# Kernel optimization log

Measured on AMD Instinct MI355X. Metric: run time of the kernel, lower is better.

The kernel has to match this reference:

```python
import jax, jax.numpy as jnp
import numpy as np

NUM_HEADS = 16
TOP_K = 64


def setup_inputs() -> dict:
    key = jax.random.key(0)
    ks = jax.random.split(key, 9)
    B, S, E = 2, 1024, 1024
    x = jax.random.normal(ks[0], (B, S, E), jnp.float32)
    init = lambda k: jax.random.normal(k, (E, E), jnp.float32) * 0.02
    return {
        "x": x,
        "Wq": init(ks[1]), "bq": jnp.zeros((E,), jnp.float32),
        "Wk": init(ks[2]), "bk": jnp.zeros((E,), jnp.float32),
        "Wv": init(ks[3]), "bv": jnp.zeros((E,), jnp.float32),
        "Wo": init(ks[4]), "bo": jnp.zeros((E,), jnp.float32),
    }


def reference(x, Wq, bq, Wk, bk, Wv, bv, Wo, bo):
    B, S, E = x.shape
    H = NUM_HEADS
    hd = E // H
    scale = jnp.sqrt(jnp.float32(hd))

    def proj(W, b):  # torch nn.Linear: y = x @ W^T + b -> [B,H,S,hd]
        return (x @ W.T + b).reshape(B, S, H, hd).transpose(0, 2, 1, 3)

    q = proj(Wq, bq)
    k = proj(Wk, bk)
    v = proj(Wv, bv)

    # full scores, then per-query top-k selection (same math as the torch per-i loop)
    scores = jnp.einsum('bhqd,bhkd->bhqk', q, k) / scale          # [B,H,S,S]
    top_scores, top_idx = jax.lax.top_k(scores, TOP_K)            # [B,H,S,K]

    # gather top-k values: vg[b,h,q,j,:] = v[b,h, top_idx[b,h,q,j], :]
    vg = jnp.take_along_axis(v[:, :, None, :, :], top_idx[..., None], axis=3)  # [B,H,S,K,hd]

    # torch recomputes q . gathered_k / scale, which equals top_scores exactly
    w = jax.nn.softmax(top_scores, axis=-1)                       # [B,H,S,K]
    out = jnp.einsum('bhqk,bhqkd->bhqd', w, vg)                   # [B,H,S,hd]

    out = out.transpose(0, 2, 1, 3).reshape(B, S, E)
    return out @ Wo.T + bo
```

## Files before the change

kernel.cpp:

```cpp
#include <hip/hip_runtime.h>
#include <hip/hip_bf16.h>
#include <stdint.h>


typedef __bf16 bf16_t;
typedef bf16_t bf16x8 __attribute__((ext_vector_type(8)));
typedef bf16_t bf16x4 __attribute__((ext_vector_type(4)));
typedef float  f32x4  __attribute__((ext_vector_type(4)));

#define NB 2
#define SS 1024
#define EE 1024
#define NH 16
#define HD 64
#define NBH (NB*NH)
#define NX_ ((size_t)NB*SS*EE)
#define NW_ ((size_t)EE*EE)

__device__ __forceinline__ f32x4 mfma16(bf16x8 a, bf16x8 b, f32x4 c) {
  return __builtin_amdgcn_mfma_f32_16x16x32_bf16(a, b, c, 0, 0, 0);
}

__device__ __forceinline__ void split3(float x, bf16_t& h, bf16_t& m, bf16_t& l) {
  h = (bf16_t)x;
  float r = x - (float)h;
  m = (bf16_t)r;
  float r2 = r - (float)m;
  l = (bf16_t)r2;
}

__device__ __forceinline__ void wave_fence() {
  __builtin_amdgcn_wave_barrier();
  __builtin_amdgcn_s_waitcnt(0);
  __builtin_amdgcn_wave_barrier();
}

__device__ __forceinline__ void gld16(const bf16_t* g, bf16_t* l) {
  __builtin_amdgcn_global_load_lds(
      (const __attribute__((address_space(1))) void*)g,
      (__attribute__((address_space(3))) void*)l, 16, 0, 0);
}

__global__ __launch_bounds__(256) void presplit_all(
    const float* __restrict__ x,  const float* __restrict__ wq,
    const float* __restrict__ wk, const float* __restrict__ wv,
    const float* __restrict__ wo, bf16_t* __restrict__ base)
{
  const int blk = blockIdx.x;
  const float* src; bf16_t* h; size_t n; int i;
  if (blk < 2048)      { src = x;  h = base;                   n = NX_; i = blk;        }
  else if (blk < 3072) { src = wq; h = base + 3*NX_;           n = NW_; i = blk - 2048; }
  else if (blk < 4096) { src = wk; h = base + 3*NX_ + 3*NW_;   n = NW_; i = blk - 3072; }
  else if (blk < 5120) { src = wv; h = base + 3*NX_ + 6*NW_;   n = NW_; i = blk - 4096; }
  else                 { src = wo; h = base + 3*NX_ + 9*NW_;   n = NW_; i = blk - 5120; }
  bf16_t* m = h + n;
  bf16_t* l = m + n;
  int idx = i * 256 + threadIdx.x;
  float4 v = ((const float4*)src)[idx];
  float t[4] = { v.x, v.y, v.z, v.w };
  bf16x4 hv, mv, lv;
#pragma unroll
  for (int j = 0; j < 4; j++) {
    bf16_t a, b, c;
    split3(t[j], a, b, c);
    hv[j] = a; mv[j] = b; lv[j] = c;
  }
  ((bf16x4*)h)[idx] = hv;
  ((bf16x4*)m)[idx] = mv;
  ((bf16x4*)l)[idx] = lv;
}

__global__ __launch_bounds__(256, 2) void gemm_qk(
    const bf16_t* __restrict__ Ah, const bf16_t* __restrict__ Am,
    const bf16_t* __restrict__ Al,
    const bf16_t* __restrict__ Bqh, const bf16_t* __restrict__ Bqm,
    const bf16_t* __restrict__ Bql,
    const bf16_t* __restrict__ Bkh, const bf16_t* __restrict__ Bkm,
    const bf16_t* __restrict__ Bkl,
    const float* __restrict__ biasq, const float* __restrict__ biask,
    bf16_t* __restrict__ qH, bf16_t* __restrict__ qM, bf16_t* __restrict__ qL,
    bf16_t* __restrict__ kH, bf16_t* __restrict__ kM, bf16_t* __restrict__ kL)
{
  __shared__ bf16_t As[3][128 * 32];
  __shared__ bf16_t Bs[3][64 * 32];

  const int z = blockIdx.z;
  const bf16_t* AP[3] = { Ah, Am, Al };
  const bf16_t* BP[3] = { z ? Bkh : Bqh, z ? Bkm : Bqm, z ? Bkl : Bql };
  const float* bias = z ? biask : biasq;
  bf16_t* dH = z ? kH : qH;
  bf16_t* dM = z ? kM : qM;
  bf16_t* dL = z ? kL : qL;

  const int tid  = threadIdx.x;
  const int wv   = tid >> 6, lane = tid & 63;
  const int quad = lane >> 4, l16 = lane & 15;
  const int m0 = blockIdx.y * 128, n0 = blockIdx.x * 64;
  const int wm = (wv & 1) * 64, wn = (wv >> 1) * 32;

  const int arow = wv * 32 + (lane >> 2);
  const int brow = wv * 16 + (lane >> 2);
  const int q8   = (lane & 3) * 8;
  const size_t aoff0 = (size_t)(m0 + arow) * 1024 + q8;
  const size_t boff  = (size_t)(n0 + brow) * 1024 + q8;

  f32x4 accH0[4][2] = {};
  f32x4 accH1[4][2] = {};
  f32x4 accC [4][2] = {};

  for (int k0 = 0; k0 < 1024; k0 += 32) {
    __syncthreads();
#pragma unroll
    for (int L = 0; L < 3; L++) {
      gld16(AP[L] + aoff0 + k0,              &As[L][(wv * 32) * 32]);
      gld16(AP[L] + aoff0 + 16 * 1024 + k0,  &As[L][(wv * 32 + 16) * 32]);
      gld16(BP[L] + boff + k0,               &Bs[L][(wv * 16) * 32]);
    }
    __syncthreads();

    bf16x8 bfr[2][3];
#pragma unroll
    for (int nt = 0; nt < 2; nt++)
#pragma unroll
      for (int L = 0; L < 3; L++)
        bfr[nt][L] = *(const bf16x8*)&Bs[L][(wn + nt * 16 + l16) * 32 + quad * 8];

    const bool hi = (k0 >= 512);
#pragma unroll
    for (int mt = 0; mt < 4; mt++) {
      bf16x8 af[3];
#pragma unroll
      for (int L = 0; L < 3; L++)
        af[L] = *(const bf16x8*)&As[L][(wm + mt * 16 + l16) * 32 + quad * 8];
#pragma unroll
      for (int nt = 0; nt < 2; nt++) {
        f32x4& H = hi ? accH1[mt][nt] : accH0[mt][nt];
        H = mfma16(af[0], bfr[nt][0], H);
        f32x4 c = accC[mt][nt];
        c = mfma16(af[0], bfr[nt][1], c);
        c = mfma16(af[1], bfr[nt][0], c);
        c = mfma16(af[0], bfr[nt][2], c);
        c = mfma16(af[2], bfr[nt][0], c);
        c = mfma16(af[1], bfr[nt][1], c);
        accC[mt][nt] = c;
      }
    }
  }

#pragma unroll
  for (int mt = 0; mt < 4; mt++)
#pragma unroll
  for (int nt = 0; nt < 2; nt++)
#pragma unroll
  for (int r  = 0; r  < 4;  r++) {
    int gm = m0 + wm + mt * 16 + quad * 4 + r;
    int gn = n0 + wn + nt * 16 + l16;
    float v = (accH0[mt][nt][r] + accH1[mt][nt][r]) + accC[mt][nt][r] + bias[gn];
    int b_ = gm >> 10, s_ = gm & 1023, h_ = gn >> 6, d_ = gn & 63;
    size_t di = (((size_t)b_ * NH + h_) * SS + s_) * HD + d_;
    bf16_t hh, mm, ll;
    split3(v, hh, mm, ll);
    dH[di] = hh; dM[di] = mm; dL[di] = ll;
  }
}

template<int MODE>
__global__ __launch_bounds__(256, 4) void gemm_nl2(
    const bf16_t* __restrict__ Ah, const bf16_t* __restrict__ Am,
    const bf16_t* __restrict__ Bh, const bf16_t* __restrict__ Bm,
    const float* __restrict__ bias, float* __restrict__ dF)
{
  __shared__ bf16_t As[2][64 * 32];
  __shared__ bf16_t Bs[2][64 * 32];

  const bf16_t* AP[2] = { Ah, Am };
  const bf16_t* BP[2] = { Bh, Bm };

  const int tid  = threadIdx.x;
  const int wv   = tid >> 6, lane = tid & 63;
  const int quad = lane >> 4, l16 = lane & 15;
  const int m0 = blockIdx.y * 64, n0 = blockIdx.x * 64;
  const int wm = (wv & 1) * 32, wn = (wv >> 1) * 32;

  const int srow = wv * 16 + (lane >> 2);
  const int q8   = (lane & 3) * 8;
  const size_t aoff = (size_t)(m0 + srow) * 1024 + q8;
  const size_t boff = (size_t)(n0 + srow) * 1024 + q8;

  f32x4 accH0[2][2] = {};
  f32x4 accH1[2][2] = {};
  f32x4 accC [2][2] = {};

  for (int k0 = 0; k0 < 1024; k0 += 32) {
    __syncthreads();
#pragma unroll
    for (int L = 0; L < 2; L++) {
      gld16(AP[L] + aoff + k0, &As[L][(wv * 16) * 32]);
      gld16(BP[L] + boff + k0, &Bs[L][(wv * 16) * 32]);
    }
    __syncthreads();

    bf16x8 bfr[2][2];
#pragma unroll
    for (int nt = 0; nt < 2; nt++)
#pragma unroll
      for (int L = 0; L < 2; L++)
        bfr[nt][L] = *(const bf16x8*)&Bs[L][(wn + nt * 16 + l16) * 32 + quad * 8];

    const bool hi = (k0 >= 512);
#pragma unroll
    for (int mt = 0; mt < 2; mt++) {
      bf16x8 af[2];
#pragma unroll
      for (int L = 0; L < 2; L++)
        af[L] = *(const bf16x8*)&As[L][(wm + mt * 16 + l16) * 32 + quad * 8];
#pragma unroll
      for (int nt = 0; nt < 2; nt++) {
        f32x4& H = hi ? accH1[mt][nt] : accH0[mt][nt];
        H = mfma16(af[0], bfr[nt][0], H);
        f32x4 c = accC[mt][nt];
        c = mfma16(af[0], bfr[nt][1], c);
        c = mfma16(af[1], bfr[nt][0], c);
        accC[mt][nt] = c;
      }
    }
  }

#pragma unroll
  for (int mt = 0; mt < 2; mt++)
#pragma unroll
  for (int nt = 0; nt < 2; nt++)
#pragma unroll
  for (int r  = 0; r  < 4;  r++) {
    int gm = m0 + wm + mt * 16 + quad * 4 + r;
    int gn = n0 + wn + nt * 16 + l16;
    float v = (accH0[mt][nt][r] + accH1[mt][nt][r]) + accC[mt][nt][r] + bias[gn];
    if (MODE == 2) {
      dF[(size_t)gm * 1024 + gn] = v;
    } else {
      int b_ = gm >> 10, s_ = gm & 1023, h_ = gn >> 6, d_ = gn & 63;
      dF[(((size_t)b_ * NH + h_) * SS + s_) * HD + d_] = v;
    }
  }
}

__global__ __launch_bounds__(1024, 4) void attn_topk(
    const bf16_t* __restrict__ qhg, const bf16_t* __restrict__ qmg,
    const bf16_t* __restrict__ qlg,
    const bf16_t* __restrict__ khg, const bf16_t* __restrict__ kmg,
    const bf16_t* __restrict__ klg,
    const float*  __restrict__ vg,
    bf16_t* __restrict__ attnH, bf16_t* __restrict__ attnM)
{
  __shared__ float  sc[16 * 516];
  __shared__ float  selW[16 * 64];
  __shared__ ushort selI[16 * 64];

  const int tid  = threadIdx.x;
  const int wv   = tid >> 6, lane = tid & 63;
  const int quad = lane >> 4, l16 = lane & 15;
  const int xcd = blockIdx.x & 7;
  const int g   = blockIdx.x >> 3;
  const int bh  = xcd + 8 * (g >> 6);
  const int qt  = g & 63;
  const int b_ = bh >> 4, h_ = bh & 15;
  const int q0 = qt * 16;

  const uint32_t qbase = ((uint32_t)bh * SS + q0 + l16) * HD + quad * 8;
  bf16x8 aH[2], aM[2], aL[2];
#pragma unroll
  for (int ks = 0; ks < 2; ks++) {
    aH[ks] = *(const bf16x8*)(qhg + qbase + ks * 32);
    aM[ks] = *(const bf16x8*)(qmg + qbase + ks * 32);
    aL[ks] = *(const bf16x8*)(qlg + qbase + ks * 32);
  }

  float fv[16];
#pragma unroll
  for (int c = 0; c < 2; c++) {
    const uint32_t kwb = ((uint32_t)bh * SS + c * 512 + wv * 32 + l16) * HD + quad * 8;
#pragma unroll
    for (int t2 = 0; t2 < 2; t2++) {
      const uint32_t kb = kwb + (uint32_t)t2 * 16 * HD;
      f32x4 accH = {}, accC = {};
      {
        bf16x8 bH = *(const bf16x8*)(khg + kb);
        bf16x8 bM = *(const bf16x8*)(kmg + kb);
        bf16x8 bL = *(const bf16x8*)(klg + kb);
        accH = mfma16(aH[0], bH, accH);
        accC = mfma16(aH[0], bM, accC);
        accC = mfma16(aM[0], bH, accC);
        accC = mfma16(aH[0], bL, accC);
        accC = mfma16(aL[0], bH, accC);
        accC = mfma16(aM[0], bM, accC);
      }
      {
        bf16x8 bH = *(const bf16x8*)(khg + kb + 32);
        bf16x8 bM = *(const bf16x8*)(kmg + kb + 32);
        bf16x8 bL = *(const bf16x8*)(klg + kb + 32);
        accH = mfma16(aH[1], bH, accH);
        accC = mfma16(aH[1], bM, accC);
        accC = mfma16(aM[1], bH, accC);
        accC = mfma16(aH[1], bL, accC);
        accC = mfma16(aL[1], bH, accC);
        accC = mfma16(aM[1], bM, accC);
      }
      int key = wv * 32 + t2 * 16 + l16;
#pragma unroll
      for (int r = 0; r < 4; r++)
        sc[(quad * 4 + r) * 516 + key] = (accH[r] + accC[r]) * 0.125f;
    }
    __syncthreads();
#pragma unroll
    for (int i = 0; i < 8; i++)
      fv[c * 8 + i] = sc[wv * 516 + i * 64 + lane];
    __syncthreads();
  }

  uint32_t* bins  = (uint32_t*)sc + wv * 516;
  float*    candV = (float*)bins;
  ushort*   candI = (ushort*)(bins + 64);

  const uint64_t lt = (1ull << lane) - 1ull;
  const int q = wv;
  {
    *(uint4*)(bins + lane * 8)     = uint4{0, 0, 0, 0};
    *(uint4*)(bins + lane * 8 + 4) = uint4{0, 0, 0, 0};
    wave_fence();
#pragma unroll
    for (int i = 0; i < 16; i++) {
      int b = (int)fmaxf(0.f, fminf(511.f, fmaf(fv[i], 32.f, 256.f)));
      atomicAdd(bins + b, 1u);
    }
    wave_fence();
    int base = 504 - 8 * lane;
    uint4 h0 = *(const uint4*)(bins + base);
    uint4 h1 = *(const uint4*)(bins + base + 4);
    uint32_t s_l = h0.x + h0.y + h0.z + h0.w + h1.x + h1.y + h1.z + h1.w;
    uint32_t x = s_l;
#pragma unroll
    for (int off = 1; off < 64; off <<= 1) {
      uint32_t y = __shfl_up(x, off);
      if (lane >= off) x += y;
    }
    uint32_t P = x - s_l;
    uint32_t harr[8] = { h1.w, h1.z, h1.y, h1.x, h0.w, h0.z, h0.y, h0.x };
    uint32_t cb = P, G = 0;
    int foundc = -1;
#pragma unroll
    for (int c = 0; c < 8; c++) {
      uint32_t hc = harr[c];
      if (foundc < 0 && (int)cb < 64 && (int)(cb + hc) >= 64) { foundc = c; G = cb; }
      cb += hc;
    }
    uint64_t fm = __ballot(foundc >= 0);
    int src   = __ffsll((unsigned long long)fm) - 1;
    int Bstar = __shfl((foundc >= 0) ? (511 - 8 * lane - foundc) : 0, src);
    int Gs    = __shfl((int)G, src);
    int needed = 64 - Gs;
    wave_fence();

    int pos = 0, cT = 0;
#pragma unroll
    for (int i = 0; i < 16; i++) {
      int b = (int)fmaxf(0.f, fminf(511.f, fmaf(fv[i], 32.f, 256.f)));
      bool hi = b > Bstar;
      bool cd = (b == Bstar);
      uint64_t hm = __ballot(hi);
      uint64_t em = __ballot(cd);
      int p  = pos + (int)__popcll(hm & lt);
      int cp = cT  + (int)__popcll(em & lt);
      if (hi) { selW[q * 64 + p] = fv[i]; selI[q * 64 + p] = (ushort)(i * 64 + lane); }
      if (cd && cp < 64) { candV[cp] = fv[i]; candI[cp] = (ushort)(i * 64 + lane); }
      pos += (int)__popcll(hm);
      cT  += (int)__popcll(em);
    }
    wave_fence();
    int C = cT < 64 ? cT : 64;
    float mv = candV[lane];
    int   mi = candI[lane];
    int rank = 0;
    for (int i = 0; i < C; i++) {
      float ov = candV[i]; int oi = candI[i];
      rank += (ov > mv || (ov == mv && oi < mi)) ? 1 : 0;
    }
    bool take = (lane < C) && (rank < needed);
    uint64_t tm = __ballot(take);
    int slot = Gs + (int)__popcll(tm & lt);
    if (take) { selW[q * 64 + slot] = mv; selI[q * 64 + slot] = (ushort)mi; }
    wave_fence();
    float sv = selW[q * 64 + lane];
    float mx = sv;
#pragma unroll
    for (int off = 32; off >= 1; off >>= 1) mx = fmaxf(mx, __shfl_xor(mx, off));
    float e = __expf(sv - mx);
    float sum = e;
#pragma unroll
    for (int off = 32; off >= 1; off >>= 1) sum += __shfl_xor(sum, off);
    selW[q * 64 + lane] = e / sum;
  }
  __syncthreads();

  {
    int q2 = tid >> 6, jq = (tid >> 4) & 3, dblk = (tid & 15) * 4;
    const float* vb = vg + (size_t)bh * SS * HD;
    f32x4 a4 = {};
    float wreg[16]; int ireg[16];
#pragma unroll
    for (int j = 0; j < 16; j++) {
      int jj = jq * 16 + j;
      wreg[j] = selW[q2 * 64 + jj];
      ireg[j] = selI[q2 * 64 + jj];
    }
#pragma unroll
    for (int j = 0; j < 16; j++) {
      f32x4 v4 = *(const f32x4*)(vb + (size_t)ireg[j] * HD + dblk);
      a4 += wreg[j] * v4;
    }
#pragma unroll
    for (int cc = 0; cc < 4; cc++) {
      a4[cc] += __shfl_xor(a4[cc], 16);
      a4[cc] += __shfl_xor(a4[cc], 32);
    }
    if (jq == 0) {
      size_t dofs = ((size_t)b_ * SS + q0 + q2) * EE + h_ * HD + dblk;
      bf16x4 oh, om;
#pragma unroll
      for (int j = 0; j < 4; j++) {
        bf16_t hh = (bf16_t)a4[j];
        oh[j] = hh;
        om[j] = (bf16_t)(a4[j] - (float)hh);
      }
      *(bf16x4*)(attnH + dofs) = oh;
      *(bf16x4*)(attnM + dofs) = om;
    }
  }
}

extern "C" void kernel_launch(void* const* d_in, const int* in_sizes, int n_in,
                              void* d_out, int out_size, void* d_ws, size_t ws_size,
                              hipStream_t stream)
{
  const float* x  = (const float*)d_in[0];
  const float* Wq = (const float*)d_in[1];
  const float* bq = (const float*)d_in[2];
  const float* Wk = (const float*)d_in[3];
  const float* bk = (const float*)d_in[4];
  const float* Wv = (const float*)d_in[5];
  const float* bv = (const float*)d_in[6];
  const float* Wo = (const float*)d_in[7];
  const float* bo = (const float*)d_in[8];

  bf16_t* base = (bf16_t*)d_ws;
  bf16_t *xh = base,            *xm = xh + NX_,  *xl = xm + NX_;
  bf16_t *wqh = base + 3*NX_,           *wqm = wqh + NW_, *wql = wqm + NW_;
  bf16_t *wkh = base + 3*NX_ + 3*NW_,   *wkm = wkh + NW_, *wkl = wkm + NW_;
  bf16_t *wvh = base + 3*NX_ + 6*NW_,   *wvm = wvh + NW_;
  bf16_t *woh = base + 3*NX_ + 9*NW_,   *wom = woh + NW_;
  bf16_t *p2 = base + 3*NX_ + 12*NW_;
  bf16_t *qh = p2,          *qm = qh + NX_, *ql = qm + NX_;
  bf16_t *kh = ql + NX_,    *km = kh + NX_, *kl = km + NX_;
  float  *vws = (float*)(kl + NX_);
  bf16_t *ath = (bf16_t*)(vws + NX_), *atm = ath + NX_;

  dim3 blk(256);
  presplit_all<<<dim3(6144), blk, 0, stream>>>(x, Wq, Wk, Wv, Wo, base);

  gemm_qk<<<dim3(EE / 64, (NB * SS) / 128, 2), blk, 0, stream>>>(
      xh, xm, xl, wqh, wqm, wql, wkh, wkm, wkl, bq, bk,
      qh, qm, ql, kh, km, kl);

  gemm_nl2<1><<<dim3(EE / 64, (NB * SS) / 64), blk, 0, stream>>>(
      xh, xm, wvh, wvm, bv, vws);

  attn_topk<<<dim3(NBH * (SS / 16)), dim3(1024), 0, stream>>>(
      qh, qm, ql, kh, km, kl, vws, ath, atm);

  gemm_nl2<2><<<dim3(EE / 64, (NB * SS) / 64), blk, 0, stream>>>(
      ath, atm, woh, wom, bo, (float*)d_out);
}
```

Before: 375.1 us.

## Halve attn_topk block to 512 threads with two queries per wave

The top-k attention kernel now runs 8 waves per block instead of 16. Each wave computes QK scores for 64 keys per chunk and handles top-k selection for two queries sequentially, and the V gather uses 32 threads per query with two batches. This is meant to lower per-block thread count and improve scheduling and occupancy on the CU. In exchange each wave carries more registers (two score vectors) and does serial selection work.

Result: faster. 330.2 us (-12.0%).

```diff
diff --git a/kernel.cpp b/kernel.cpp
--- a/kernel.cpp
+++ b/kernel.cpp
@@ -244,7 +244,7 @@
   }
 }
 
-__global__ __launch_bounds__(1024, 4) void attn_topk(
+__global__ __launch_bounds__(512, 4) void attn_topk(
     const bf16_t* __restrict__ qhg, const bf16_t* __restrict__ qmg,
     const bf16_t* __restrict__ qlg,
     const bf16_t* __restrict__ khg, const bf16_t* __restrict__ kmg,
@@ -275,12 +275,12 @@
     aL[ks] = *(const bf16x8*)(qlg + qbase + ks * 32);
   }
 
-  float fv[16];
+  float fv[2][16];
 #pragma unroll
   for (int c = 0; c < 2; c++) {
-    const uint32_t kwb = ((uint32_t)bh * SS + c * 512 + wv * 32 + l16) * HD + quad * 8;
-#pragma unroll
-    for (int t2 = 0; t2 < 2; t2++) {
+    const uint32_t kwb = ((uint32_t)bh * SS + c * 512 + wv * 64 + l16) * HD + quad * 8;
+#pragma unroll
+    for (int t2 = 0; t2 < 4; t2++) {
       const uint32_t kb = kwb + (uint32_t)t2 * 16 * HD;
       f32x4 accH = {}, accC = {};
       {
@@ -305,15 +305,17 @@
         accC = mfma16(aL[1], bH, accC);
         accC = mfma16(aM[1], bM, accC);
       }
-      int key = wv * 32 + t2 * 16 + l16;
+      int key = wv * 64 + t2 * 16 + l16;
 #pragma unroll
       for (int r = 0; r < 4; r++)
         sc[(quad * 4 + r) * 516 + key] = (accH[r] + accC[r]) * 0.125f;
     }
     __syncthreads();
 #pragma unroll
-    for (int i = 0; i < 8; i++)
-      fv[c * 8 + i] = sc[wv * 516 + i * 64 + lane];
+    for (int i = 0; i < 8; i++) {
+      fv[0][c * 8 + i] = sc[wv * 516 + i * 64 + lane];
+      fv[1][c * 8 + i] = sc[(wv + 8) * 516 + i * 64 + lane];
+    }
     __syncthreads();
   }
 
@@ -322,14 +324,15 @@
   ushort*   candI = (ushort*)(bins + 64);
 
   const uint64_t lt = (1ull << lane) - 1ull;
-  const int q = wv;
-  {
+  for (int qi = 0; qi < 2; qi++) {
+    int q = qi * 8 + wv;
+    const float* fq = fv[qi];
     *(uint4*)(bins + lane * 8)     = uint4{0, 0, 0, 0};
     *(uint4*)(bins + lane * 8 + 4) = uint4{0, 0, 0, 0};
     wave_fence();
 #pragma unroll
     for (int i = 0; i < 16; i++) {
-      int b = (int)fmaxf(0.f, fminf(511.f, fmaf(fv[i], 32.f, 256.f)));
+      int b = (int)fmaxf(0.f, fminf(511.f, fmaf(fq[i], 32.f, 256.f)));
       atomicAdd(bins + b, 1u);
     }
     wave_fence();
@@ -363,15 +366,15 @@
     int pos = 0, cT = 0;
 #pragma unroll
     for (int i = 0; i < 16; i++) {
-      int b = (int)fmaxf(0.f, fminf(511.f, fmaf(fv[i], 32.f, 256.f)));
+      int b = (int)fmaxf(0.f, fminf(511.f, fmaf(fq[i], 32.f, 256.f)));
       bool hi = b > Bstar;
       bool cd = (b == Bstar);
       uint64_t hm = __ballot(hi);
       uint64_t em = __ballot(cd);
       int p  = pos + (int)__popcll(hm & lt);
       int cp = cT  + (int)__popcll(em & lt);
-      if (hi) { selW[q * 64 + p] = fv[i]; selI[q * 64 + p] = (ushort)(i * 64 + lane); }
-      if (cd && cp < 64) { candV[cp] = fv[i]; candI[cp] = (ushort)(i * 64 + lane); }
+      if (hi) { selW[q * 64 + p] = fq[i]; selI[q * 64 + p] = (ushort)(i * 64 + lane); }
+      if (cd && cp < 64) { candV[cp] = fq[i]; candI[cp] = (ushort)(i * 64 + lane); }
       pos += (int)__popcll(hm);
       cT  += (int)__popcll(em);
     }
@@ -398,32 +401,33 @@
 #pragma unroll
     for (int off = 32; off >= 1; off >>= 1) sum += __shfl_xor(sum, off);
     selW[q * 64 + lane] = e / sum;
+    wave_fence();
   }
   __syncthreads();
 
   {
-    int q2 = tid >> 6, jq = (tid >> 4) & 3, dblk = (tid & 15) * 4;
+    int q = tid >> 5, jh = (tid >> 4) & 1, dblk = (tid & 15) * 4;
     const float* vb = vg + (size_t)bh * SS * HD;
     f32x4 a4 = {};
-    float wreg[16]; int ireg[16];
-#pragma unroll
-    for (int j = 0; j < 16; j++) {
-      int jj = jq * 16 + j;
-      wreg[j] = selW[q2 * 64 + jj];
-      ireg[j] = selI[q2 * 64 + jj];
-    }
-#pragma unroll
-    for (int j = 0; j < 16; j++) {
-      f32x4 v4 = *(const f32x4*)(vb + (size_t)ireg[j] * HD + dblk);
-      a4 += wreg[j] * v4;
-    }
-#pragma unroll
-    for (int cc = 0; cc < 4; cc++) {
-      a4[cc] += __shfl_xor(a4[cc], 16);
-      a4[cc] += __shfl_xor(a4[cc], 32);
-    }
-    if (jq == 0) {
-      size_t dofs = ((size_t)b_ * SS + q0 + q2) * EE + h_ * HD + dblk;
+#pragma unroll
+    for (int bch = 0; bch < 2; bch++) {
+      float wreg[16]; int ireg[16];
+#pragma unroll
+      for (int j = 0; j < 16; j++) {
+        int jj = jh * 32 + bch * 16 + j;
+        wreg[j] = selW[q * 64 + jj];
+        ireg[j] = selI[q * 64 + jj];
+      }
+#pragma unroll
+      for (int j = 0; j < 16; j++) {
+        f32x4 v4 = *(const f32x4*)(vb + (size_t)ireg[j] * HD + dblk);
+        a4 += wreg[j] * v4;
+      }
+    }
+#pragma unroll
+    for (int c = 0; c < 4; c++) a4[c] += __shfl_xor(a4[c], 16);
+    if (jh == 0) {
+      size_t dofs = ((size_t)b_ * SS + q0 + q) * EE + h_ * HD + dblk;
       bf16x4 oh, om;
 #pragma unroll
       for (int j = 0; j < 4; j++) {
@@ -473,7 +477,7 @@
   gemm_nl2<1><<<dim3(EE / 64, (NB * SS) / 64), blk, 0, stream>>>(
       xh, xm, wvh, wvm, bv, vws);
 
-  attn_topk<<<dim3(NBH * (SS / 16)), dim3(1024), 0, stream>>>(
+  attn_topk<<<dim3(NBH * (SS / 16)), dim3(512), 0, stream>>>(
       qh, qm, ql, kh, km, kl, vws, ath, atm);
 
   gemm_nl2<2><<<dim3(EE / 64, (NB * SS) / 64), blk, 0, stream>>>(
```
